# Performance work log

Measured on AMD Instinct MI355X. Metric: run time of the kernel, lower is better.

## Reference

```python
import jax, jax.numpy as jnp
import numpy as np

N_NODES = 50000
N_EDGES = 800000
N_GRAPHS = 64
IN_CH = 128
HID_CH = 128
FC_CH = 128


def setup_inputs() -> dict:
    key = jax.random.key(0)
    ks = jax.random.split(key, 12)

    def lin_w(k, fan_in, fan_out):
        return jax.random.normal(k, (fan_in, fan_out), jnp.float32) * (1.0 / np.sqrt(fan_in))

    return {
        "x": jax.random.normal(ks[0], (N_NODES, IN_CH), jnp.float32),
        "edge_index": jax.random.randint(ks[1], (2, N_EDGES), 0, N_NODES, dtype=jnp.int64),
        "batch_vec": jnp.sort(jax.random.randint(ks[2], (N_NODES,), 0, N_GRAPHS, dtype=jnp.int64)),
        "W1": lin_w(ks[3], IN_CH, HID_CH),
        "b1": jnp.zeros((HID_CH,), jnp.float32),
        "W2": lin_w(ks[4], HID_CH, HID_CH),
        "b2": jnp.zeros((HID_CH,), jnp.float32),
        "W3": lin_w(ks[5], HID_CH, FC_CH),
        "b3": jnp.zeros((FC_CH,), jnp.float32),
        "fcW1": lin_w(ks[6], FC_CH, IN_CH),
        "fcb1": jnp.zeros((IN_CH,), jnp.float32),
        "fcW2": lin_w(ks[7], IN_CH, 2),
        "fcb2": jnp.zeros((2,), jnp.float32),
    }


def reference(x, edge_index, batch_vec, W1, b1, W2, b2, W3, b3, fcW1, fcb1, fcW2, fcb2):
    n = x.shape[0]
    row, col = edge_index[0], edge_index[1]  # src -> dst

    # GCN symmetric normalization with self-loops: deg[j] = in-degree(j) + 1
    deg = jnp.zeros((n,), x.dtype).at[col].add(1.0) + 1.0
    inv_sqrt = jax.lax.rsqrt(deg)
    edge_norm = inv_sqrt[row] * inv_sqrt[col]  # [E]
    self_norm = (inv_sqrt * inv_sqrt)[:, None]  # [N,1], self-loop weight 1/deg

    def gcn(h, W, b):
        h = h @ W  # [N, out]
        agg = jnp.zeros_like(h).at[col].add(h[row] * edge_norm[:, None])
        return agg + h * self_norm + b

    h = jax.nn.relu(gcn(x, W1, b1))
    h = jax.nn.relu(gcn(h, W2, b2))
    h = jax.nn.relu(gcn(h, W3, b3))
    h = jax.nn.relu(h @ fcW1 + fcb1)
    h = h @ fcW2 + fcb2  # [N, 2]

    # global mean pool per graph
    sums = jax.ops.segment_sum(h, batch_vec, num_segments=N_GRAPHS)
    cnts = jax.ops.segment_sum(jnp.ones((n,), h.dtype), batch_vec, num_segments=N_GRAPHS)
    pooled = sums / jnp.maximum(cnts, 1.0)[:, None]  # [G, 2]
    return jax.nn.softmax(pooled, axis=1)
```

## Files before the change

### kernel.cpp

```cpp
#include <hip/hip_runtime.h>


#define CH 128
#define BSH 7
#define SEG 4096
#define EPW 4096
#define SA 40
#define SC 132
#define SC8 144

typedef unsigned short ushortT;
typedef unsigned int uintT;
typedef unsigned char ucharT;
typedef __attribute__((ext_vector_type(8))) short short8;
typedef __attribute__((ext_vector_type(4))) float floatx4;
typedef __attribute__((ext_vector_type(2))) float floatx2;

__device__ __forceinline__ float bf2f(uintT u) {
    return __uint_as_float(u << 16);
}
__device__ __forceinline__ ushortT f2bf(float f) {
    uintT x = __float_as_uint(f);
    return (ushortT)((x + 0x7fffu + ((x >> 16) & 1u)) >> 16);
}

__global__ void k_zero(int* __restrict__ bfill, int NB, float* __restrict__ acc, int nacc) {
    int t = threadIdx.x;
    for (int i = t; i < NB; i += 256) bfill[i] = 0;
    for (int i = t; i < nacc; i += 256) acc[i] = 0.f;
}

__global__ __launch_bounds__(256) void k_bin(const int* __restrict__ row,
                                             const int* __restrict__ col,
                                             int* __restrict__ bfill,
                                             uintT* __restrict__ seg,
                                             int E, int NB) {
    __shared__ uintT staged[EPW];
    __shared__ int target[EPW];
    __shared__ int sval[512];
    __shared__ int horig[512];
    __shared__ int pcnt[512];
    __shared__ int gbase[512];
    const int t = threadIdx.x;
    const int e0 = blockIdx.x * EPW;
    const int cnt = min(EPW, E - e0);

    sval[t] = 0; sval[t + 256] = 0;
    __syncthreads();

    int er[16], ec[16];
#pragma unroll
    for (int i = 0; i < 16; ++i) {
        int le = i * 256 + t;
        if (le < cnt) {
            er[i] = row[e0 + le];
            ec[i] = col[e0 + le];
            atomicAdd(&sval[ec[i] >> BSH], 1);
        }
    }
    __syncthreads();
    horig[t] = sval[t]; horig[t + 256] = sval[t + 256];
    __syncthreads();
    for (int off = 1; off < 512; off <<= 1) {
        int a = (t >= off) ? sval[t - off] : 0;
        int b2 = sval[t + 256 - off];
        __syncthreads();
        sval[t] += a;
        sval[t + 256] += b2;
        __syncthreads();
    }
    for (int b = t; b < 512; b += 256) {
        int h = horig[b];
        pcnt[b] = sval[b] - h;
        gbase[b] = (h > 0 && b < NB) ? atomicAdd(&bfill[b], h) : 0;
    }
    __syncthreads();
#pragma unroll
    for (int i = 0; i < 16; ++i) {
        int le = i * 256 + t;
        if (le < cnt) {
            int b = ec[i] >> BSH;
            int j = atomicAdd(&pcnt[b], 1);
            staged[j] = (uintT)er[i] | ((uintT)ec[i] << 16);
            int lo = sval[b] - horig[b];
            target[j] = b * SEG + gbase[b] + (j - lo);
        }
    }
    __syncthreads();
    for (int s = t; s < cnt; s += 256) seg[target[s]] = staged[s];
}

__global__ __launch_bounds__(512) void k_binvs_bscan(const int* __restrict__ bfill,
                                                     const uintT* __restrict__ seg,
                                                     float* __restrict__ invs,
                                                     int* __restrict__ bbase,
                                                     int* __restrict__ indptr,
                                                     int NB, int N, int E) {
    const int b = blockIdx.x;
    const int t = threadIdx.x;
    if (b < NB) {
        __shared__ int h[128];
        if (t < 128) h[t] = 0;
        __syncthreads();
        int cnt = bfill[b];
        const uintT* sp = seg + (size_t)b * SEG;
        for (int s = t; s < cnt; s += 512) atomicAdd(&h[(sp[s] >> 16) & 127], 1);
        __syncthreads();
        int d = b * 128 + t;
        if (t < 128 && d < N) invs[d] = rsqrtf((float)h[t] + 1.0f);
    } else {
        __shared__ int s[512];
        int v = (t < NB) ? bfill[t] : 0;
        s[t] = v;
        __syncthreads();
        for (int off = 1; off < 512; off <<= 1) {
            int a = (t >= off) ? s[t - off] : 0;
            __syncthreads();
            s[t] += a;
            __syncthreads();
        }
        if (t < NB) bbase[t] = s[t] - v;
        if (t == 0) indptr[N] = E;
    }
}

__global__ __launch_bounds__(256) void k_scatterprep(const int* __restrict__ bfill,
                                                     const int* __restrict__ bbase,
                                                     const uintT* __restrict__ seg,
                                                     const float* __restrict__ invs,
                                                     int* __restrict__ indptr,
                                                     uintT* __restrict__ epack,
                                                     const float* __restrict__ X,
                                                     ucharT* __restrict__ Xb,
                                                     const float* __restrict__ w0,
                                                     const float* __restrict__ w1,
                                                     const float* __restrict__ w2,
                                                     const float* __restrict__ w3,
                                                     ushortT* __restrict__ Whi,
                                                     int N, int NB, int total4) {
    const int t = threadIdx.x;
    if ((int)blockIdx.x < NB) {
        __shared__ uintT staged[SEG];
        __shared__ int h[128];
        __shared__ int sc[128];
        __shared__ int pc[128];
        const int b = blockIdx.x;
        const int cnt = bfill[b];
        const int base = bbase[b];
        const uintT* sp = seg + (size_t)b * SEG;

        if (t < 128) h[t] = 0;
        __syncthreads();
        for (int s = t; s < cnt; s += 256) atomicAdd(&h[(sp[s] >> 16) & 127], 1);
        __syncthreads();
        if (t < 128) sc[t] = h[t];
        __syncthreads();
        for (int off = 1; off < 128; off <<= 1) {
            int a = (t >= off && t < 128) ? sc[t - off] : 0;
            __syncthreads();
            if (t < 128) sc[t] += a;
            __syncthreads();
        }
        if (t < 128) {
            int excl = sc[t] - h[t];
            pc[t] = excl;
            int d = b * 128 + t;
            if (d < N) indptr[d] = base + excl;
        }
        __syncthreads();
        for (int s = t; s < cnt; s += 256) {
            uintT rc = sp[s];
            int src = (int)(rc & 0xffffu), dst = (int)(rc >> 16);
            int j = atomicAdd(&pc[dst & 127], 1);
            float nrm = invs[src] * invs[dst];
            staged[j] = (uintT)src | ((uintT)f2bf(nrm) << 16);
        }
        __syncthreads();
        for (int s = t; s < cnt; s += 256) epack[base + s] = staged[s];
    } else if ((int)blockIdx.x < NB + 256) {
        int idx = (blockIdx.x - NB) * 256 + t;
        int m = idx >> 14;
        int r = idx & 16383;
        int n = r >> 7;
        int k = r & 127;
        const float* W = (m == 0) ? w0 : (m == 1) ? w1 : (m == 2) ? w2 : w3;
        Whi[m * 16384 + n * CH + k] = f2bf(W[k * CH + n]);
    } else {
        int i = (blockIdx.x - NB - 256) * 256 + t;
        if (i < total4) {
            float4 v = reinterpret_cast<const float4*>(X)[i];
            int r0 = __builtin_amdgcn_cvt_pk_fp8_f32(v.x, v.y, 0, false);
            int r1 = __builtin_amdgcn_cvt_pk_fp8_f32(v.z, v.w, r0, true);
            reinterpret_cast<int*>(Xb)[i] = r1;
        }
    }
}

__global__ __launch_bounds__(256) void k_agg(const ucharT* __restrict__ H8,
                                             const uintT* __restrict__ epack,
                                             const int* __restrict__ indptr,
                                             const float* __restrict__ invs,
                                             ushortT* __restrict__ Zb, int N) {
    int node = blockIdx.x * 4 + (threadIdx.x >> 6);
    if (node >= N) return;
    int lane = threadIdx.x & 63;

    const ushortT* H16 = reinterpret_cast<const ushortT*>(H8);

    float sn = invs[node];
    float sn2 = sn * sn;
    floatx2 hf = __builtin_amdgcn_cvt_pk_f32_fp8((int)H16[(size_t)node * 64 + lane], false);
    float ax = sn2 * hf.x, ay = sn2 * hf.y;

    int p = indptr[node];
    int p1 = indptr[node + 1];
    for (; p + 8 <= p1; p += 8) {
        uintT e[8];
#pragma unroll
        for (int i = 0; i < 8; ++i) e[i] = epack[p + i];
        uintT g[8];
#pragma unroll
        for (int i = 0; i < 8; ++i) g[i] = H16[(size_t)(int)(e[i] & 0xffffu) * 64 + lane];
#pragma unroll
        for (int i = 0; i < 8; ++i) {
            float wv = bf2f(e[i] >> 16);
            floatx2 gf = __builtin_amdgcn_cvt_pk_f32_fp8((int)g[i], false);
            ax += wv * gf.x;
            ay += wv * gf.y;
        }
    }
    if (p + 4 <= p1) {
        uintT e[4];
#pragma unroll
        for (int i = 0; i < 4; ++i) e[i] = epack[p + i];
        uintT g[4];
#pragma unroll
        for (int i = 0; i < 4; ++i) g[i] = H16[(size_t)(int)(e[i] & 0xffffu) * 64 + lane];
#pragma unroll
        for (int i = 0; i < 4; ++i) {
            float wv = bf2f(e[i] >> 16);
            floatx2 gf = __builtin_amdgcn_cvt_pk_f32_fp8((int)g[i], false);
            ax += wv * gf.x;
            ay += wv * gf.y;
        }
        p += 4;
    }
    for (; p < p1; ++p) {
        uintT e = epack[p];
        uintT g = H16[(size_t)(int)(e & 0xffffu) * 64 + lane];
        float wv = bf2f(e >> 16);
        floatx2 gf = __builtin_amdgcn_cvt_pk_f32_fp8((int)g, false);
        ax += wv * gf.x;
        ay += wv * gf.y;
    }
    uintT o = (uintT)f2bf(ax) | ((uintT)f2bf(ay) << 16);
    reinterpret_cast<uintT*>(Zb)[(size_t)node * 64 + lane] = o;
}

__global__ __launch_bounds__(256) void k_gemm(const ushortT* __restrict__ Zg,
                                              const ushortT* __restrict__ Whi,
                                              const float* __restrict__ Bias,
                                              void* __restrict__ OutV, int N,
                                              int outFp8) {
    __shared__ ushortT smem[128 * SC];
    ushortT* As = smem;
    ushortT* Ws = smem + 128 * SA;
    ushortT* Cs = smem;

    const int tid = threadIdx.x;
    const int wave = tid >> 6, lane = tid & 63;
    const int quad = lane >> 4, l15 = lane & 15;
    const int mBase = (wave >> 1) * 64, nBase = (wave & 1) * 64;
    const int row0 = blockIdx.x * 128;
    const int r = tid >> 1, half = tid & 1;

    floatx4 acc[4][4];
    const floatx4 zero4 = {0.f, 0.f, 0.f, 0.f};
#pragma unroll
    for (int i = 0; i < 4; i++)
#pragma unroll
        for (int j = 0; j < 4; j++) acc[i][j] = zero4;

    for (int ks = 0; ks < 4; ++ks) {
        {
            int grow = row0 + r;
            uint4 av0 = {0, 0, 0, 0}, av1 = {0, 0, 0, 0};
            if (grow < N) {
                const uint4* s = reinterpret_cast<const uint4*>(
                    Zg + (size_t)grow * CH + ks * 32 + half * 16);
                av0 = s[0]; av1 = s[1];
            }
            uint4* d = reinterpret_cast<uint4*>(&As[r * SA + half * 16]);
            d[0] = av0; d[1] = av1;
            const uint4* sh = reinterpret_cast<const uint4*>(Whi + r * CH + ks * 32 + half * 16);
            uint4* dh = reinterpret_cast<uint4*>(&Ws[r * SA + half * 16]);
            dh[0] = sh[0]; dh[1] = sh[1];
        }
        __syncthreads();

        short8 af[4], wf[4];
#pragma unroll
        for (int mt = 0; mt < 4; ++mt)
            af[mt] = *reinterpret_cast<const short8*>(&As[(mBase + mt * 16 + l15) * SA + quad * 8]);
#pragma unroll
        for (int nt = 0; nt < 4; ++nt)
            wf[nt] = *reinterpret_cast<const short8*>(&Ws[(nBase + nt * 16 + l15) * SA + quad * 8]);
#pragma unroll
        for (int mt = 0; mt < 4; ++mt)
#pragma unroll
            for (int nt = 0; nt < 4; ++nt)
                acc[mt][nt] = __builtin_amdgcn_mfma_f32_16x16x32_bf16(af[mt], wf[nt], acc[mt][nt], 0, 0, 0);
        __syncthreads();
    }

    float bb[4];
#pragma unroll
    for (int nt = 0; nt < 4; ++nt) bb[nt] = Bias[nBase + nt * 16 + l15];

    if (outFp8) {
        ucharT* Cs8 = reinterpret_cast<ucharT*>(Cs);
#pragma unroll
        for (int mt = 0; mt < 4; ++mt)
#pragma unroll
            for (int nt = 0; nt < 4; ++nt)
#pragma unroll
                for (int r4 = 0; r4 < 4; ++r4) {
                    int lrow = mBase + mt * 16 + quad * 4 + r4;
                    float v = fmaxf(acc[mt][nt][r4] + bb[nt], 0.f);
                    int f8 = __builtin_amdgcn_cvt_pk_fp8_f32(v, 0.f, 0, false);
                    Cs8[lrow * SC8 + nBase + nt * 16 + l15] = (ucharT)(f8 & 0xff);
                }
        __syncthreads();
        int grow = row0 + r;
        if (grow < N) {
            const uint4* s4 = reinterpret_cast<const uint4*>(&Cs8[r * SC8 + half * 64]);
            uint4* dst = reinterpret_cast<uint4*>((ucharT*)OutV + (size_t)grow * CH + half * 64);
#pragma unroll
            for (int q = 0; q < 4; ++q) dst[q] = s4[q];
        }
    } else {
        ushortT* Out = (ushortT*)OutV;
#pragma unroll
        for (int mt = 0; mt < 4; ++mt)
#pragma unroll
            for (int nt = 0; nt < 4; ++nt)
#pragma unroll
                for (int r4 = 0; r4 < 4; ++r4) {
                    int lrow = mBase + mt * 16 + quad * 4 + r4;
                    float v = fmaxf(acc[mt][nt][r4] + bb[nt], 0.f);
                    Cs[lrow * SC + nBase + nt * 16 + l15] = f2bf(v);
                }
        __syncthreads();
        int grow = row0 + r;
        if (grow < N) {
            const uint2* s = reinterpret_cast<const uint2*>(&Cs[r * SC + half * 64]);
            uint4* dst = reinterpret_cast<uint4*>(Out + (size_t)grow * CH + half * 64);
#pragma unroll
            for (int q = 0; q < 8; ++q) {
                uint2 a = s[2 * q], b = s[2 * q + 1];
                uint4 o = {a.x, a.y, b.x, b.y};
                dst[q] = o;
            }
        }
    }
}

__global__ __launch_bounds__(256) void k_fc2pool(const ushortT* __restrict__ H,
                                                 const float* __restrict__ W2,
                                                 const float* __restrict__ B2,
                                                 const int* __restrict__ batch,
                                                 float* __restrict__ sums,
                                                 float* __restrict__ cnts, int N) {
    __shared__ float ls[192];
    const int t = threadIdx.x;
    if (t < 192) ls[t] = 0.f;
    __syncthreads();
    const int wave = t >> 6, lane = t & 63;
    const int sub = lane & 7;
    const int ng = lane >> 3;

    float w0[16], w1[16];
#pragma unroll
    for (int i = 0; i < 16; ++i) {
        float2 wv = *reinterpret_cast<const float2*>(W2 + (sub * 16 + i) * 2);
        w0[i] = wv.x;
        w1[i] = wv.y;
    }
    const float b0 = B2[0], b1 = B2[1];

    const int nodeBase = blockIdx.x * 256 + wave * 64;
#pragma unroll
    for (int it = 0; it < 8; ++it) {
        int node = nodeBase + it * 8 + ng;
        float d0 = 0.f, d1 = 0.f;
        if (node < N) {
            const uint4* hp = reinterpret_cast<const uint4*>(H + (size_t)node * CH + sub * 16);
            uint4 a = hp[0], b = hp[1];
            uintT uu[8] = {a.x, a.y, a.z, a.w, b.x, b.y, b.z, b.w};
#pragma unroll
            for (int q = 0; q < 8; ++q) {
                float h0 = bf2f(uu[q] & 0xffffu);
                float h1 = bf2f(uu[q] >> 16);
                d0 += h0 * w0[2 * q] + h1 * w0[2 * q + 1];
                d1 += h0 * w1[2 * q] + h1 * w1[2 * q + 1];
            }
        }
#pragma unroll
        for (int m = 4; m >= 1; m >>= 1) {
            d0 += __shfl_xor(d0, m, 64);
            d1 += __shfl_xor(d1, m, 64);
        }
        if (sub == 0 && node < N) {
            int g = batch[node];
            atomicAdd(&ls[g], d0 + b0);
            atomicAdd(&ls[64 + g], d1 + b1);
            atomicAdd(&ls[128 + g], 1.0f);
        }
    }
    __syncthreads();
    if (t < 64) {
        float c = ls[128 + t];
        if (c != 0.f) {
            atomicAdd(&sums[2 * t], ls[t]);
            atomicAdd(&sums[2 * t + 1], ls[64 + t]);
            atomicAdd(&cnts[t], c);
        }
    }
}

__global__ void k_softmax(const float* __restrict__ sums, const float* __restrict__ cnts,
                          float* __restrict__ out, int G) {
    int g = blockIdx.x * blockDim.x + threadIdx.x;
    if (g < G) {
        float c = fmaxf(cnts[g], 1.0f);
        float p0 = sums[2 * g] / c;
        float p1 = sums[2 * g + 1] / c;
        float m = fmaxf(p0, p1);
        float e0 = expf(p0 - m), e1 = expf(p1 - m);
        float inv = 1.f / (e0 + e1);
        out[2 * g] = e0 * inv;
        out[2 * g + 1] = e1 * inv;
    }
}

extern "C" void kernel_launch(void* const* d_in, const int* in_sizes, int n_in,
                              void* d_out, int out_size, void* d_ws, size_t ws_size,
                              hipStream_t stream) {
    const float* X   = (const float*)d_in[0];
    const int* EI    = (const int*)d_in[1];
    const int* BATCH = (const int*)d_in[2];
    const float* W1  = (const float*)d_in[3];
    const float* B1  = (const float*)d_in[4];
    const float* W2  = (const float*)d_in[5];
    const float* B2  = (const float*)d_in[6];
    const float* W3  = (const float*)d_in[7];
    const float* B3  = (const float*)d_in[8];
    const float* FW1 = (const float*)d_in[9];
    const float* FB1 = (const float*)d_in[10];
    const float* FW2 = (const float*)d_in[11];
    const float* FB2 = (const float*)d_in[12];

    const int N = in_sizes[0] / CH;
    const int E = in_sizes[1] / 2;
    const int G = out_size / 2;
    const int* rowp = EI;
    const int* colp = EI + E;
    const int NB = (N + 127) >> BSH;

    char* w = (char*)d_ws;
    auto alloc = [&](size_t bytes) -> char* {
        char* p = w;
        w += (bytes + 255) & ~(size_t)255;
        return p;
    };
    ushortT* Zb    = (ushortT*)alloc((size_t)N * CH * 2);
    ushortT* Hb16  = (ushortT*)alloc((size_t)N * CH * 2);
    ucharT*  Hb8   = (ucharT*)alloc((size_t)N * CH);
    ucharT*  Xb8   = (ucharT*)alloc((size_t)N * CH);
    ushortT* WhiA  = (ushortT*)alloc((size_t)4 * 16384 * 2);
    float* invs    = (float*)alloc((size_t)N * 4);
    int*   indptr  = (int*)alloc((size_t)(N + 1) * 4);
    uintT* epack   = (uintT*)alloc((size_t)E * 4);
    uintT* seg     = (uintT*)alloc((size_t)NB * SEG * 4);
    int*   bfill   = (int*)alloc((size_t)NB * 4);
    int*   bbase   = (int*)alloc((size_t)NB * 4);
    float* sums    = (float*)alloc((size_t)G * 3 * 4);
    float* cnts    = sums + 2 * G;

    const int nbAgg  = (N + 3) / 4;
    const int nbGemm = (N + 127) / 128;
    const int nbBin  = (E + EPW - 1) / EPW;
    const int nbPool = (N + 255) / 256;
    const int total4 = N * CH / 4;
    const int nbSP   = NB + 256 + (total4 + 255) / 256;

    k_zero<<<1, 256, 0, stream>>>(bfill, NB, sums, 3 * G);
    k_bin<<<nbBin, 256, 0, stream>>>(rowp, colp, bfill, seg, E, NB);
    k_binvs_bscan<<<NB + 1, 512, 0, stream>>>(bfill, seg, invs, bbase, indptr, NB, N, E);
    k_scatterprep<<<nbSP, 256, 0, stream>>>(bfill, bbase, seg, invs, indptr, epack,
                                            X, Xb8, W1, W2, W3, FW1, WhiA, N, NB, total4);

    k_agg<<<nbAgg, 256, 0, stream>>>(Xb8, epack, indptr, invs, Zb, N);
    k_gemm<<<nbGemm, 256, 0, stream>>>(Zb, WhiA, B1, Hb8, N, 1);
    k_agg<<<nbAgg, 256, 0, stream>>>(Hb8, epack, indptr, invs, Zb, N);
    k_gemm<<<nbGemm, 256, 0, stream>>>(Zb, WhiA + 16384, B2, Hb8, N, 1);
    k_agg<<<nbAgg, 256, 0, stream>>>(Hb8, epack, indptr, invs, Zb, N);
    k_gemm<<<nbGemm, 256, 0, stream>>>(Zb, WhiA + 2 * 16384, B3, Hb16, N, 0);
    k_gemm<<<nbGemm, 256, 0, stream>>>(Hb16, WhiA + 3 * 16384, FB1, Zb, N, 0);
    k_fc2pool<<<nbPool, 256, 0, stream>>>(Zb, FW2, FB2, BATCH, sums, cnts, N);
    k_softmax<<<1, 64, 0, stream>>>(sums, cnts, (float*)d_out, G);
}
```

Baseline: 252.8 us.

## Store aggregation output as fp8 and widen agg to 16 lanes per node

```diff
diff --git a/kernel.cpp b/kernel.cpp
--- a/kernel.cpp
+++ b/kernel.cpp
@@ -22,6 +22,11 @@
 __device__ __forceinline__ ushortT f2bf(float f) {
     uintT x = __float_as_uint(f);
     return (ushortT)((x + 0x7fffu + ((x >> 16) & 1u)) >> 16);
+}
+__device__ __forceinline__ void dec4(uintT u, float* o) {
+    floatx2 lo = __builtin_amdgcn_cvt_pk_f32_fp8((int)u, false);
+    floatx2 hi = __builtin_amdgcn_cvt_pk_f32_fp8((int)u, true);
+    o[0] = lo.x; o[1] = lo.y; o[2] = hi.x; o[3] = hi.y;
 }
 
 __global__ void k_zero(int* __restrict__ bfill, int NB, float* __restrict__ acc, int nacc) {
@@ -200,17 +205,25 @@
                                              const uintT* __restrict__ epack,
                                              const int* __restrict__ indptr,
                                              const float* __restrict__ invs,
-                                             ushortT* __restrict__ Zb, int N) {
-    int node = blockIdx.x * 4 + (threadIdx.x >> 6);
+                                             ucharT* __restrict__ Z8, int N) {
+    const int wave = threadIdx.x >> 6, lane = threadIdx.x & 63;
+    const int sub = lane >> 4;
+    const int l = lane & 15;
+    const int node = blockIdx.x * 16 + wave * 4 + sub;
     if (node >= N) return;
-    int lane = threadIdx.x & 63;
-
-    const ushortT* H16 = reinterpret_cast<const ushortT*>(H8);
-
-    float sn = invs[node];
-    float sn2 = sn * sn;
-    floatx2 hf = __builtin_amdgcn_cvt_pk_f32_fp8((int)H16[(size_t)node * 64 + lane], false);
-    float ax = sn2 * hf.x, ay = sn2 * hf.y;
+
+    const uint2* H2 = reinterpret_cast<const uint2*>(H8);
+
+    float acc[8];
+    {
+        float sn = invs[node];
+        float sn2 = sn * sn;
+        uint2 h = H2[(size_t)node * 16 + l];
+        float d[8];
+        dec4(h.x, d); dec4(h.y, d + 4);
+#pragma unroll
+        for (int j = 0; j < 8; ++j) acc[j] = sn2 * d[j];
+    }
 
     int p = indptr[node];
     int p1 = indptr[node + 1];
@@ -218,50 +231,61 @@
         uintT e[8];
 #pragma unroll
         for (int i = 0; i < 8; ++i) e[i] = epack[p + i];
-        uintT g[8];
-#pragma unroll
-        for (int i = 0; i < 8; ++i) g[i] = H16[(size_t)(int)(e[i] & 0xffffu) * 64 + lane];
+        uint2 g[8];
+#pragma unroll
+        for (int i = 0; i < 8; ++i) g[i] = H2[(size_t)(int)(e[i] & 0xffffu) * 16 + l];
 #pragma unroll
         for (int i = 0; i < 8; ++i) {
             float wv = bf2f(e[i] >> 16);
-            floatx2 gf = __builtin_amdgcn_cvt_pk_f32_fp8((int)g[i], false);
-            ax += wv * gf.x;
-            ay += wv * gf.y;
+            float d[8];
+            dec4(g[i].x, d); dec4(g[i].y, d + 4);
+#pragma unroll
+            for (int j = 0; j < 8; ++j) acc[j] += wv * d[j];
         }
     }
     if (p + 4 <= p1) {
         uintT e[4];
 #pragma unroll
         for (int i = 0; i < 4; ++i) e[i] = epack[p + i];
-        uintT g[4];
-#pragma unroll
-        for (int i = 0; i < 4; ++i) g[i] = H16[(size_t)(int)(e[i] & 0xffffu) * 64 + lane];
+        uint2 g[4];
+#pragma unroll
+        for (int i = 0; i < 4; ++i) g[i] = H2[(size_t)(int)(e[i] & 0xffffu) * 16 + l];
 #pragma unroll
         for (int i = 0; i < 4; ++i) {
             float wv = bf2f(e[i] >> 16);
-            floatx2 gf = __builtin_amdgcn_cvt_pk_f32_fp8((int)g[i], false);
-            ax += wv * gf.x;
-            ay += wv * gf.y;
+            float d[8];
+            dec4(g[i].x, d); dec4(g[i].y, d + 4);
+#pragma unroll
+            for (int j = 0; j < 8; ++j) acc[j] += wv * d[j];
         }
         p += 4;
     }
     for (; p < p1; ++p) {
         uintT e = epack[p];
-        uintT g = H16[(size_t)(int)(e & 0xffffu) * 64 + lane];
+        uint2 g = H2[(size_t)(int)(e & 0xffffu) * 16 + l];
         float wv = bf2f(e >> 16);
-        floatx2 gf = __builtin_amdgcn_cvt_pk_f32_fp8((int)g, false);
-        ax += wv * gf.x;
-        ay += wv * gf.y;
-    }
-    uintT o = (uintT)f2bf(ax) | ((uintT)f2bf(ay) << 16);
-    reinterpret_cast<uintT*>(Zb)[(size_t)node * 64 + lane] = o;
-}
-
-__global__ __launch_bounds__(256) void k_gemm(const ushortT* __restrict__ Zg,
+        float d[8];
+        dec4(g.x, d); dec4(g.y, d + 4);
+#pragma unroll
+        for (int j = 0; j < 8; ++j) acc[j] += wv * d[j];
+    }
+
+    uint2 o;
+    {
+        int r0 = __builtin_amdgcn_cvt_pk_fp8_f32(acc[0], acc[1], 0, false);
+        r0 = __builtin_amdgcn_cvt_pk_fp8_f32(acc[2], acc[3], r0, true);
+        int r1 = __builtin_amdgcn_cvt_pk_fp8_f32(acc[4], acc[5], 0, false);
+        r1 = __builtin_amdgcn_cvt_pk_fp8_f32(acc[6], acc[7], r1, true);
+        o.x = (uintT)r0; o.y = (uintT)r1;
+    }
+    reinterpret_cast<uint2*>(Z8)[(size_t)node * 16 + l] = o;
+}
+
+__global__ __launch_bounds__(256) void k_gemm(const void* __restrict__ InV,
                                               const ushortT* __restrict__ Whi,
                                               const float* __restrict__ Bias,
                                               void* __restrict__ OutV, int N,
-                                              int outFp8) {
+                                              int inFp8, int outFp8) {
     __shared__ ushortT smem[128 * SC];
     ushortT* As = smem;
     ushortT* Ws = smem + 128 * SA;
@@ -284,14 +308,33 @@
     for (int ks = 0; ks < 4; ++ks) {
         {
             int grow = row0 + r;
-            uint4 av0 = {0, 0, 0, 0}, av1 = {0, 0, 0, 0};
-            if (grow < N) {
-                const uint4* s = reinterpret_cast<const uint4*>(
-                    Zg + (size_t)grow * CH + ks * 32 + half * 16);
-                av0 = s[0]; av1 = s[1];
+            if (inFp8) {
+                uint4 a8 = {0, 0, 0, 0};
+                if (grow < N)
+                    a8 = *reinterpret_cast<const uint4*>(
+                        (const ucharT*)InV + (size_t)grow * CH + ks * 32 + half * 16);
+                uintT wds[4] = {a8.x, a8.y, a8.z, a8.w};
+                uintT ob[8];
+#pragma unroll
+                for (int q = 0; q < 4; ++q) {
+                    float d[4];
+                    dec4(wds[q], d);
+                    ob[2 * q] = (uintT)f2bf(d[0]) | ((uintT)f2bf(d[1]) << 16);
+                    ob[2 * q + 1] = (uintT)f2bf(d[2]) | ((uintT)f2bf(d[3]) << 16);
+                }
+                uint4* dd = reinterpret_cast<uint4*>(&As[r * SA + half * 16]);
+                dd[0] = uint4{ob[0], ob[1], ob[2], ob[3]};
+                dd[1] = uint4{ob[4], ob[5], ob[6], ob[7]};
+            } else {
+                uint4 av0 = {0, 0, 0, 0}, av1 = {0, 0, 0, 0};
+                if (grow < N) {
+                    const uint4* s = reinterpret_cast<const uint4*>(
+                        (const ushortT*)InV + (size_t)grow * CH + ks * 32 + half * 16);
+                    av0 = s[0]; av1 = s[1];
+                }
+                uint4* d = reinterpret_cast<uint4*>(&As[r * SA + half * 16]);
+                d[0] = av0; d[1] = av1;
             }
-            uint4* d = reinterpret_cast<uint4*>(&As[r * SA + half * 16]);
-            d[0] = av0; d[1] = av1;
             const uint4* sh = reinterpret_cast<const uint4*>(Whi + r * CH + ks * 32 + half * 16);
             uint4* dh = reinterpret_cast<uint4*>(&Ws[r * SA + half * 16]);
             dh[0] = sh[0]; dh[1] = sh[1];
@@ -475,6 +518,7 @@
     };
     ushortT* Zb    = (ushortT*)alloc((size_t)N * CH * 2);
     ushortT* Hb16  = (ushortT*)alloc((size_t)N * CH * 2);
+    ucharT*  Z8    = (ucharT*)alloc((size_t)N * CH);
     ucharT*  Hb8   = (ucharT*)alloc((size_t)N * CH);
     ucharT*  Xb8   = (ucharT*)alloc((size_t)N * CH);
     ushortT* WhiA  = (ushortT*)alloc((size_t)4 * 16384 * 2);
@@ -487,7 +531,7 @@
     float* sums    = (float*)alloc((size_t)G * 3 * 4);
     float* cnts    = sums + 2 * G;
 
-    const int nbAgg  = (N + 3) / 4;
+    const int nbAgg  = (N + 15) / 16;
     const int nbGemm = (N + 127) / 128;
     const int nbBin  = (E + EPW - 1) / EPW;
     const int nbPool = (N + 255) / 256;
@@ -500,13 +544,13 @@
     k_scatterprep<<<nbSP, 256, 0, stream>>>(bfill, bbase, seg, invs, indptr, epack,
                                             X, Xb8, W1, W2, W3, FW1, WhiA, N, NB, total4);
 
-    k_agg<<<nbAgg, 256, 0, stream>>>(Xb8, epack, indptr, invs, Zb, N);
-    k_gemm<<<nbGemm, 256, 0, stream>>>(Zb, WhiA, B1, Hb8, N, 1);
-    k_agg<<<nbAgg, 256, 0, stream>>>(Hb8, epack, indptr, invs, Zb, N);
-    k_gemm<<<nbGemm, 256, 0, stream>>>(Zb, WhiA + 16384, B2, Hb8, N, 1);
-    k_agg<<<nbAgg, 256, 0, stream>>>(Hb8, epack, indptr, invs, Zb, N);
-    k_gemm<<<nbGemm, 256, 0, stream>>>(Zb, WhiA + 2 * 16384, B3, Hb16, N, 0);
-    k_gemm<<<nbGemm, 256, 0, stream>>>(Hb16, WhiA + 3 * 16384, FB1, Zb, N, 0);
+    k_agg<<<nbAgg, 256, 0, stream>>>(Xb8, epack, indptr, invs, Z8, N);
+    k_gemm<<<nbGemm, 256, 0, stream>>>(Z8, WhiA, B1, Hb8, N, 1, 1);
+    k_agg<<<nbAgg, 256, 0, stream>>>(Hb8, epack, indptr, invs, Z8, N);
+    k_gemm<<<nbGemm, 256, 0, stream>>>(Z8, WhiA + 16384, B2, Hb8, N, 1, 1);
+    k_agg<<<nbAgg, 256, 0, stream>>>(Hb8, epack, indptr, invs, Z8, N);
+    k_gemm<<<nbGemm, 256, 0, stream>>>(Z8, WhiA + 2 * 16384, B3, Hb16, N, 1, 0);
+    k_gemm<<<nbGemm, 256, 0, stream>>>(Hb16, WhiA + 3 * 16384, FB1, Zb, N, 0, 0);
     k_fc2pool<<<nbPool, 256, 0, stream>>>(Zb, FW2, FB2, BATCH, sums, cnts, N);
     k_softmax<<<1, 64, 0, stream>>>(sums, cnts, (float*)d_out, G);
 }
```

Measured after the change: 228.0 us. -9.8%, faster.
